# Performance work log

Hardware: AMD Instinct MI355X
Metric: run time of the kernel (lower is better)

The kernel has to match this reference:

```python
import jax, jax.numpy as jnp
import numpy as np

H_RES, W_RES = 32, 32
DIM = 512
NUM_HEADS = 16
HEAD_DIM = DIM // NUM_HEADS
SCALE = HEAD_DIM ** -0.5
B = 16
N = H_RES * W_RES
TABLE_SIZE = (2 * H_RES - 1) * (2 * W_RES - 1)


def _relative_position_index():
    coords_h = np.arange(H_RES)
    coords_w = np.arange(W_RES)
    coords = np.stack(np.meshgrid(coords_h, coords_w, indexing='ij'))  # [2, H, W]
    coords_flat = coords.reshape(2, -1)  # [2, N]
    rel = coords_flat[:, :, None] - coords_flat[:, None, :]  # [2, N, N]
    rel = rel.transpose(1, 2, 0).astype(np.int64)  # [N, N, 2]
    rel[:, :, 0] += H_RES - 1
    rel[:, :, 1] += W_RES - 1
    rel[:, :, 0] *= 2 * W_RES - 1
    return rel.sum(-1)  # [N, N]


def setup_inputs() -> dict:
    key = jax.random.key(0)
    ks = jax.random.split(key, 6)
    x = jax.random.normal(ks[0], (B, N, DIM), dtype=jnp.float32)
    w_qkv = jax.random.normal(ks[1], (DIM, 3 * DIM), dtype=jnp.float32) * (DIM ** -0.5)
    b_qkv = jnp.zeros((3 * DIM,), dtype=jnp.float32)
    w_proj = jax.random.normal(ks[2], (DIM, DIM), dtype=jnp.float32) * (DIM ** -0.5)
    b_proj = jnp.zeros((DIM,), dtype=jnp.float32)
    bias_table = jax.random.normal(ks[3], (TABLE_SIZE, NUM_HEADS), dtype=jnp.float32) * 0.02
    rel_index = jnp.asarray(_relative_position_index(), dtype=jnp.int32)
    return {"x": x, "w_qkv": w_qkv, "b_qkv": b_qkv, "w_proj": w_proj,
            "b_proj": b_proj, "bias_table": bias_table, "rel_index": rel_index}


def reference(x, w_qkv, b_qkv, w_proj, b_proj, bias_table, rel_index):
    Bq, Nq, C = x.shape
    qkv = x @ w_qkv + b_qkv  # [B, N, 3C]
    qkv = qkv.reshape(Bq, Nq, 3, NUM_HEADS, HEAD_DIM)
    q = qkv[:, :, 0].transpose(0, 2, 1, 3) * SCALE  # [B, nH, N, d]
    k = qkv[:, :, 1].transpose(0, 2, 1, 3)
    v = qkv[:, :, 2].transpose(0, 2, 1, 3)
    attn = jnp.einsum('bhnd,bhmd->bhnm', q, k)  # [B, nH, N, N]
    bias = bias_table[rel_index]  # [N, N, nH]
    attn = attn + bias.transpose(2, 0, 1)[None]  # broadcast over batch
    attn = jax.nn.softmax(attn, axis=-1)
    out = jnp.einsum('bhnm,bhmd->bhnd', attn, v)  # [B, nH, N, d]
    out = out.transpose(0, 2, 1, 3).reshape(Bq, Nq, C)
    return out @ w_proj + b_proj
```

## Files before the change

### kernel.cpp

```cpp
#include <hip/hip_runtime.h>
#include <hip/hip_bf16.h>
#include <cstdint>
#include <cstddef>

typedef _Float16 f16;
typedef __attribute__((ext_vector_type(8))) _Float16 f16x8;
typedef __attribute__((ext_vector_type(4))) _Float16 f16x4v;
typedef __bf16 bf16;
typedef __attribute__((ext_vector_type(4))) float f32x4;
typedef __attribute__((ext_vector_type(16))) float f32x16;

#define LOG2E 1.4426950408889634f
#define QK_SCALE 0.17677669529663687f

__device__ __forceinline__ f32x4 mfma16f(f16x8 a, f16x8 b, f32x4 c) {
  return __builtin_amdgcn_mfma_f32_16x16x32_f16(a, b, c, 0, 0, 0);
}
__device__ __forceinline__ f32x16 mfma32f(f16x8 a, f16x8 b, f32x16 c) {
  return __builtin_amdgcn_mfma_f32_32x32x16_f16(a, b, c, 0, 0, 0);
}
__device__ __forceinline__ float exp2_hw(float x) {
  float r; asm("v_exp_f32 %0, %1" : "=v"(r) : "v"(x)); return r;
}
__device__ __forceinline__ uint32_t cvtpk_f16(float a, float b) {
  uint32_t r; asm("v_cvt_pkrtz_f16_f32 %0, %1, %2" : "=v"(r) : "v"(a), "v"(b)); return r;
}
__device__ __forceinline__ void pl32swap(uint32_t& a, uint32_t& b) {
  asm("v_permlane32_swap_b32 %0, %1" : "+v"(a), "+v"(b));
}
__device__ __forceinline__ float lo16f(uint32_t u) { return __uint_as_float(u << 16); }
__device__ __forceinline__ float hi16f(uint32_t u) { return __uint_as_float(u & 0xFFFF0000u); }

__device__ __forceinline__ uint32_t packoff(int m, int k) {
  return (((uint32_t)(m >> 7) * 16u + (uint32_t)(k >> 5)) * 8u + (uint32_t)((m >> 4) & 7)) * 512u
       + (uint32_t)((k >> 3) & 3) * 128u + (uint32_t)(m & 15) * 8u + (uint32_t)(k & 7);
}

__global__ __launch_bounds__(256) void prep_kernel(
    const float* __restrict__ x, const float* __restrict__ wqkv, const float* __restrict__ wproj,
    f16* __restrict__ Xp, f16* __restrict__ Wq, f16* __restrict__ Wp)
{
  const int X4 = 16384 * 512 / 4;
  int e = blockIdx.x * 256 + threadIdx.x;
  if (e < X4) {
    int m = e >> 7, k4 = e & 127;
    f32x4 v = *(const f32x4*)(x + (size_t)e * 4);
    f16x4v o;
    #pragma unroll
    for (int j = 0; j < 4; ++j) o[j] = (f16)v[j];
    *(f16x4v*)(Xp + packoff(m, k4 * 4)) = o;
  } else if (e < X4 + 1536 * 512) {
    int e2 = e - X4;
    int n = e2 >> 9, k = e2 & 511;
    Wq[packoff(n, k)] = (f16)wqkv[k * 1536 + n];
  } else {
    int e3 = e - (X4 + 1536 * 512);
    if (e3 < 512 * 512) {
      int n = e3 >> 9, k = e3 & 511;
      Wp[packoff(n, k)] = (f16)wproj[k * 512 + n];
    }
  }
}

__global__ __launch_bounds__(256) void tblT_kernel(
    const float* __restrict__ btab, float* __restrict__ tblT)
{
  int e = blockIdx.x * 256 + threadIdx.x;
  if (e < 3969 * 16) {
    int h = e & 15, i = e >> 4;
    tblT[h * 4000 + i] = btab[e] * LOG2E;
  }
}

__global__ __launch_bounds__(256) void bias_kernel(
    const float* __restrict__ tblT, bf16* __restrict__ biasM)
{
  int t = blockIdx.x * 256 + threadIdx.x;
  int lane = t & 63;
  int kvb  = (t >> 6) & 31;
  int qb   = (t >> 11) & 31;
  int h    = t >> 16;
  int lq = lane & 31, hi5 = lane >> 5;
  int q = qb * 32 + lq;
  int base = ((q >> 5) + 31) * 63 + (q & 31) + 31 - kvb * 63;
  const float* tp = tblT + h * 4000 + base;
  bf16 outv[16];
  #pragma unroll
  for (int r = 0; r < 16; ++r) {
    int s = (r & 3) + 8 * (r >> 2) + 4 * hi5;
    outv[r] = (bf16)tp[-s];
  }
  *(uint4*)(biasM + (size_t)t * 16) = *(uint4*)&outv[0];
  *(uint4*)(biasM + (size_t)t * 16 + 8) = *(uint4*)&outv[8];
}

template<int NB>
__global__ __launch_bounds__(256) void gemm_frag(
    const f16* __restrict__ Ap, const f16* __restrict__ Bp,
    const float* __restrict__ bvec,
    f16* __restrict__ Qp, f16* __restrict__ Kp, f16* __restrict__ Vt,
    float* __restrict__ out)
{
  const int bid = blockIdx.x;
  const int xcd = bid & 7, idx = bid >> 3;
  int mb, nb;
  if (NB == 12) { int q = idx / 12; mb = xcd * 16 + q; nb = idx - q * 12; }
  else          { mb = xcd * 16 + (idx >> 2); nb = idx & 3; }
  const int tid = threadIdx.x, lane = tid & 63, wave = tid >> 6;
  const int l15 = lane & 15, l4 = lane >> 4;
  const int wr = wave >> 1, wc = wave & 1;

  const f16* pA = Ap + (uint32_t)mb * 65536u + (uint32_t)wr * 2048u + (uint32_t)lane * 8u;
  const f16* pB = Bp + (uint32_t)nb * 65536u + (uint32_t)wc * 2048u + (uint32_t)lane * 8u;

  f16x8 aA[4], bA[4], aB[4], bB[4];
  #pragma unroll
  for (int f = 0; f < 4; ++f) {
    aA[f] = *(const f16x8*)(pA + f * 512);
    bA[f] = *(const f16x8*)(pB + f * 512);
  }
  __builtin_amdgcn_sched_barrier(0);
  #pragma unroll
  for (int f = 0; f < 4; ++f) {
    aB[f] = *(const f16x8*)(pA + 4096 + f * 512);
    bB[f] = *(const f16x8*)(pB + 4096 + f * 512);
  }
  __builtin_amdgcn_sched_barrier(0);
  pA += 8192; pB += 8192;

  f32x4 acc[4][4];
  #pragma unroll
  for (int i = 0; i < 4; ++i)
    #pragma unroll
    for (int j = 0; j < 4; ++j) acc[i][j] = (f32x4){0.f, 0.f, 0.f, 0.f};

  #pragma unroll 1
  for (int it = 0; it < 8; ++it) {
    asm volatile("s_waitcnt vmcnt(8)" ::: "memory");
    #pragma unroll
    for (int mf = 0; mf < 4; ++mf)
      #pragma unroll
      for (int nf = 0; nf < 4; ++nf)
        acc[mf][nf] = mfma16f(aA[mf], bA[nf], acc[mf][nf]);
    #pragma unroll
    for (int f = 0; f < 4; ++f) {
      aA[f] = *(const f16x8*)(pA + f * 512);
      bA[f] = *(const f16x8*)(pB + f * 512);
    }
    __builtin_amdgcn_sched_barrier(0);
    asm volatile("s_waitcnt vmcnt(8)" ::: "memory");
    #pragma unroll
    for (int mf = 0; mf < 4; ++mf)
      #pragma unroll
      for (int nf = 0; nf < 4; ++nf)
        acc[mf][nf] = mfma16f(aB[mf], bB[nf], acc[mf][nf]);
    #pragma unroll
    for (int f = 0; f < 4; ++f) {
      aB[f] = *(const f16x8*)(pA + 4096 + f * 512);
      bB[f] = *(const f16x8*)(pB + 4096 + f * 512);
    }
    __builtin_amdgcn_sched_barrier(0);
    pA += 8192; pB += 8192;
  }

  #pragma unroll
  for (int mf = 0; mf < 4; ++mf) {
    #pragma unroll
    for (int nf = 0; nf < 4; ++nf) {
      int colb = nb * 128 + wc * 64 + nf * 16 + l15;
      float bb = bvec[colb];
      #pragma unroll
      for (int i = 0; i < 4; ++i) {
        int m = mb * 128 + wr * 64 + mf * 16 + l4 * 4 + i;
        float v = acc[mf][nf][i] + bb;
        if (NB == 4) {
          out[(size_t)m * 512 + colb] = v;
        } else {
          int t = colb >> 9, cc = colb & 511;
          int b = m >> 10, n = m & 1023;
          int hh = cc >> 5, d = cc & 31;
          int bh2 = b * 16 + hh;
          if (t == 0) {
            v *= (QK_SCALE * LOG2E);
            uint32_t off = (((uint32_t)bh2 * 32u + (uint32_t)(n >> 5)) * 2u + (uint32_t)(d >> 4)) * 512u
                         + ((uint32_t)((d >> 3) & 1) * 32u + (uint32_t)(n & 31)) * 8u + (uint32_t)(d & 7);
            Qp[off] = (f16)v;
          } else if (t == 1) {
            Kp[((size_t)(bh2 * 2 + (d >> 4)) * 1024 + n) * 16 + (d & 15)] = (f16)v;
          } else {
            Vt[((size_t)(bh2 * 128 + (n >> 3)) * 32 + d) * 8 + (n & 7)] = (f16)v;
          }
        }
      }
    }
  }
}

__global__ __launch_bounds__(256) void attn_kernel(
    const f16* __restrict__ Qp, const f16* __restrict__ Kp, const f16* __restrict__ Vt,
    const bf16* __restrict__ biasM, f16* __restrict__ Op)
{
  const int bid = blockIdx.x;
  const int xcd = bid & 7, slot = bid >> 3;
  const int h = xcd * 2 + (slot >> 6);
  const int rest = slot & 63;
  const int qg = rest >> 4, b = rest & 15;
  const int bh = b * 16 + h;
  const int tid = threadIdx.x, lane = tid & 63, wave = tid >> 6;
  const int lq = lane & 31, hi5 = lane >> 5;

  const int qb0 = qg * 8 + wave * 2;
  const int m0 = b * 1024 + qb0 * 32;

  const uint32_t qbase = ((uint32_t)bh * 32u + (uint32_t)qb0) * 1024u + (uint32_t)lane * 8u;
  const f16x8 q00 = *(const f16x8*)(Qp + qbase);
  const f16x8 q01 = *(const f16x8*)(Qp + qbase + 512);
  const f16x8 q10 = *(const f16x8*)(Qp + qbase + 1024);
  const f16x8 q11 = *(const f16x8*)(Qp + qbase + 1536);

  uint32_t koff = (uint32_t)bh * 32768u + (uint32_t)lq * 16u + (uint32_t)hi5 * 8u;
  uint32_t voff = (uint32_t)bh * 32768u + (uint32_t)hi5 * 256u + (uint32_t)lq * 8u;
  uint32_t boff = ((uint32_t)h * 32u + (uint32_t)qb0) * 32768u + (uint32_t)lane * 16u;

  f16x8 kA0 = *(const f16x8*)(Kp + koff);
  f16x8 kA1 = *(const f16x8*)(Kp + koff + 16384);
  uint4 p0A = *(const uint4*)(biasM + boff);
  uint4 p1A = *(const uint4*)(biasM + boff + 8);
  uint4 p2A = *(const uint4*)(biasM + boff + 32768);
  uint4 p3A = *(const uint4*)(biasM + boff + 32768 + 8);
  f16x8 vA0 = *(const f16x8*)(Vt + voff);
  f16x8 vA1 = *(const f16x8*)(Vt + voff + 512);
  f16x8 kB0 = *(const f16x8*)(Kp + koff + 512);
  f16x8 kB1 = *(const f16x8*)(Kp + koff + 16384 + 512);
  uint4 p0B = *(const uint4*)(biasM + boff + 1024);
  uint4 p1B = *(const uint4*)(biasM + boff + 1024 + 8);
  uint4 p2B = *(const uint4*)(biasM + boff + 32768 + 1024);
  uint4 p3B = *(const uint4*)(biasM + boff + 32768 + 1024 + 8);
  f16x8 vB0 = *(const f16x8*)(Vt + voff + 1024);
  f16x8 vB1 = *(const f16x8*)(Vt + voff + 1536);

  f32x16 O0, O1;
  #pragma unroll
  for (int i = 0; i < 16; ++i) { O0[i] = 0.f; O1[i] = 0.f; }
  f32x4 racc0 = {0.f, 0.f, 0.f, 0.f}, racc1 = {0.f, 0.f, 0.f, 0.f};

  union Uf { uint32_t u[4]; f16x8 v; };

#define UNPACK16(S, Pa, Pb)                              \
  S[0]  = lo16f(Pa.x); S[1]  = hi16f(Pa.x);              \
  S[2]  = lo16f(Pa.y); S[3]  = hi16f(Pa.y);              \
  S[4]  = lo16f(Pa.z); S[5]  = hi16f(Pa.z);              \
  S[6]  = lo16f(Pa.w); S[7]  = hi16f(Pa.w);              \
  S[8]  = lo16f(Pb.x); S[9]  = hi16f(Pb.x);              \
  S[10] = lo16f(Pb.y); S[11] = hi16f(Pb.y);              \
  S[12] = lo16f(Pb.z); S[13] = hi16f(Pb.z);              \
  S[14] = lo16f(Pb.w); S[15] = hi16f(Pb.w);

  auto tile = [&](f16x8& K0, f16x8& K1, f16x8& V0, f16x8& V1,
                  uint4& P0, uint4& P1, uint4& P2, uint4& P3,
                  uint32_t kpre, uint32_t vpre, uint32_t bpre) {
    asm volatile("s_waitcnt vmcnt(8)" ::: "memory");
    f32x16 S0, S1;
    UNPACK16(S0, P0, P1)
    UNPACK16(S1, P2, P3)
    S0 = mfma32f(K0, q00, S0);
    S0 = mfma32f(K1, q01, S0);
    S1 = mfma32f(K0, q10, S1);
    S1 = mfma32f(K1, q11, S1);
    K0 = *(const f16x8*)(Kp + koff + kpre);
    K1 = *(const f16x8*)(Kp + koff + 16384 + kpre);
    P0 = *(const uint4*)(biasM + boff + bpre);
    P1 = *(const uint4*)(biasM + boff + bpre + 8);
    P2 = *(const uint4*)(biasM + boff + 32768 + bpre);
    P3 = *(const uint4*)(biasM + boff + 32768 + bpre + 8);
    __builtin_amdgcn_sched_barrier(0);
    {
      float e0  = exp2_hw(S0[0]),  e1  = exp2_hw(S0[1]),  e2  = exp2_hw(S0[2]),  e3  = exp2_hw(S0[3]);
      float e4  = exp2_hw(S0[4]),  e5  = exp2_hw(S0[5]),  e6  = exp2_hw(S0[6]),  e7  = exp2_hw(S0[7]);
      float e8  = exp2_hw(S0[8]),  e9  = exp2_hw(S0[9]),  e10 = exp2_hw(S0[10]), e11 = exp2_hw(S0[11]);
      float e12 = exp2_hw(S0[12]), e13 = exp2_hw(S0[13]), e14 = exp2_hw(S0[14]), e15 = exp2_hw(S0[15]);
      racc0[0] += e0 + e4;   racc0[1] += e1 + e5;
      racc0[2] += e2 + e6;   racc0[3] += e3 + e7;
      racc0[0] += e8 + e12;  racc0[1] += e9 + e13;
      racc0[2] += e10 + e14; racc0[3] += e11 + e15;
      uint32_t u0 = cvtpk_f16(e0,  e1),  u1 = cvtpk_f16(e2,  e3);
      uint32_t u2 = cvtpk_f16(e4,  e5),  u3 = cvtpk_f16(e6,  e7);
      uint32_t u4 = cvtpk_f16(e8,  e9),  u5 = cvtpk_f16(e10, e11);
      uint32_t u6 = cvtpk_f16(e12, e13), u7 = cvtpk_f16(e14, e15);
      pl32swap(u0, u2); pl32swap(u1, u3); pl32swap(u4, u6); pl32swap(u5, u7);
      Uf a1; a1.u[0] = u0; a1.u[1] = u1; a1.u[2] = u2; a1.u[3] = u3;
      Uf a2; a2.u[0] = u4; a2.u[1] = u5; a2.u[2] = u6; a2.u[3] = u7;
      O0 = mfma32f(a1.v, V0, O0);
      O0 = mfma32f(a2.v, V1, O0);
    }
    {
      float e0  = exp2_hw(S1[0]),  e1  = exp2_hw(S1[1]),  e2  = exp2_hw(S1[2]),  e3  = exp2_hw(S1[3]);
      float e4  = exp2_hw(S1[4]),  e5  = exp2_hw(S1[5]),  e6  = exp2_hw(S1[6]),  e7  = exp2_hw(S1[7]);
      float e8  = exp2_hw(S1[8]),  e9  = exp2_hw(S1[9]),  e10 = exp2_hw(S1[10]), e11 = exp2_hw(S1[11]);
      float e12 = exp2_hw(S1[12]), e13 = exp2_hw(S1[13]), e14 = exp2_hw(S1[14]), e15 = exp2_hw(S1[15]);
      racc1[0] += e0 + e4;   racc1[1] += e1 + e5;
      racc1[2] += e2 + e6;   racc1[3] += e3 + e7;
      racc1[0] += e8 + e12;  racc1[1] += e9 + e13;
      racc1[2] += e10 + e14; racc1[3] += e11 + e15;
      uint32_t u0 = cvtpk_f16(e0,  e1),  u1 = cvtpk_f16(e2,  e3);
      uint32_t u2 = cvtpk_f16(e4,  e5),  u3 = cvtpk_f16(e6,  e7);
      uint32_t u4 = cvtpk_f16(e8,  e9),  u5 = cvtpk_f16(e10, e11);
      uint32_t u6 = cvtpk_f16(e12, e13), u7 = cvtpk_f16(e14, e15);
      pl32swap(u0, u2); pl32swap(u1, u3); pl32swap(u4, u6); pl32swap(u5, u7);
      Uf a1; a1.u[0] = u0; a1.u[1] = u1; a1.u[2] = u2; a1.u[3] = u3;
      Uf a2; a2.u[0] = u4; a2.u[1] = u5; a2.u[2] = u6; a2.u[3] = u7;
      O1 = mfma32f(a1.v, V0, O1);
      O1 = mfma32f(a2.v, V1, O1);
    }
    V0 = *(const f16x8*)(Vt + voff + vpre);
    V1 = *(const f16x8*)(Vt + voff + vpre + 512);
    __builtin_amdgcn_sched_barrier(0);
  };

  #pragma unroll 1
  for (int it = 0; it < 16; ++it) {
    tile(kA0, kA1, vA0, vA1, p0A, p1A, p2A, p3A, 1024u, 2048u, 2048u);
    tile(kB0, kB1, vB0, vB1, p0B, p1B, p2B, p3B, 1536u, 3072u, 3072u);
    koff += 1024u; voff += 2048u; boff += 2048u;
  }

  float rs0 = (racc0[0] + racc0[1]) + (racc0[2] + racc0[3]);
  rs0 += __shfl_xor(rs0, 32);
  float inv0 = 1.0f / rs0;
  float rs1 = (racc1[0] + racc1[1]) + (racc1[2] + racc1[3]);
  rs1 += __shfl_xor(rs1, 32);
  float inv1 = 1.0f / rs1;

  const int kcol = h * 32 + lq;
  #pragma unroll
  for (int r = 0; r < 16; ++r) {
    int qrow = (r & 3) + 8 * (r >> 2) + 4 * hi5;
    float t0 = __shfl(inv0, qrow);
    float t1 = __shfl(inv1, qrow);
    Op[packoff(m0 + qrow, kcol)] = (f16)(O0[r] * t0);
    Op[packoff(m0 + 32 + qrow, kcol)] = (f16)(O1[r] * t1);
  }
}

extern "C" void kernel_launch(void* const* d_in, const int* in_sizes, int n_in,
                              void* d_out, int out_size, void* d_ws, size_t ws_size,
                              hipStream_t stream) {
  const float* x     = (const float*)d_in[0];
  const float* wqkv  = (const float*)d_in[1];
  const float* bqkv  = (const float*)d_in[2];
  const float* wproj = (const float*)d_in[3];
  const float* bproj = (const float*)d_in[4];
  const float* btab  = (const float*)d_in[5];
  float* out = (float*)d_out;

  char* ws = (char*)d_ws;
  size_t off = 0;
  auto walloc = [&](size_t bytes) {
    void* p = ws + off;
    off += (bytes + 255) & ~(size_t)255;
    return p;
  };
  const size_t PAD = 262144;
  f16* Xp   = (f16*)walloc((size_t)16384 * 512 * 2 + PAD);
  f16* Wq   = (f16*)walloc((size_t)1536 * 512 * 2 + PAD);
  f16* Wp   = (f16*)walloc((size_t)512 * 512 * 2 + PAD);
  float* tblT = (float*)walloc((size_t)16 * 4000 * 4);
  f16* Qp   = (f16*)walloc((size_t)16384 * 512 * 2 + PAD);
  f16* Kp   = (f16*)walloc((size_t)16384 * 512 * 2 + PAD);
  f16* Vt   = (f16*)walloc((size_t)16384 * 512 * 2 + PAD);
  bf16* biasM = (bf16*)walloc((size_t)16 * 1024 * 1024 * 2 + PAD);
  f16* Op   = (f16*)walloc((size_t)16384 * 512 * 2 + PAD);

  const int prep_total = 16384 * 512 / 4 + 1536 * 512 + 512 * 512;
  prep_kernel<<<(prep_total + 255) / 256, 256, 0, stream>>>(
      x, wqkv, wproj, Xp, Wq, Wp);

  tblT_kernel<<<(3969 * 16 + 255) / 256, 256, 0, stream>>>(btab, tblT);

  bias_kernel<<<4096, 256, 0, stream>>>(tblT, biasM);

  gemm_frag<12><<<1536, 256, 0, stream>>>(
      Xp, Wq, bqkv, Qp, Kp, Vt, nullptr);

  attn_kernel<<<1024, 256, 0, stream>>>(Qp, Kp, Vt, biasM, Op);

  gemm_frag<4><<<512, 256, 0, stream>>>(
      Op, Wp, bproj, nullptr, nullptr, nullptr, out);
}
```

Baseline: 181.3 us.

## Compress bias to Toeplitz rows, LDS-stage GEMM, and MFMA row sums

Three changes land together. The full per-head N×N bias matrix (32 MB bf16) is replaced by a compact table of 63 block-diagonal slices per head, which the attention kernel indexes with a decreasing pointer, so bias reads come from a small, cache-resident buffer instead of HBM. The GEMM now stages A and B tiles through a triple-buffered LDS ring using global_load_lds, with barriers, instead of direct register loads. The softmax row sums are computed by extra MFMAs against a ones vector rather than VALU adds and shuffles. The costs are extra LDS barriers in the GEMM and doubled MFMA work for the row sums.

Result: faster. 169.7 us (-6.4%).

```diff
diff --git a/kernel.cpp b/kernel.cpp
--- a/kernel.cpp
+++ b/kernel.cpp
@@ -30,6 +30,12 @@
 }
 __device__ __forceinline__ float lo16f(uint32_t u) { return __uint_as_float(u << 16); }
 __device__ __forceinline__ float hi16f(uint32_t u) { return __uint_as_float(u & 0xFFFF0000u); }
+
+__device__ __forceinline__ void gl16(const f16* g, f16* l) {
+  __builtin_amdgcn_global_load_lds(
+      (const __attribute__((address_space(1))) void*)g,
+      (__attribute__((address_space(3))) void*)l, 16, 0, 0);
+}
 
 __device__ __forceinline__ uint32_t packoff(int m, int k) {
   return (((uint32_t)(m >> 7) * 16u + (uint32_t)(k >> 5)) * 8u + (uint32_t)((m >> 4) & 7)) * 512u
@@ -72,26 +78,24 @@
   }
 }
 
-__global__ __launch_bounds__(256) void bias_kernel(
-    const float* __restrict__ tblT, bf16* __restrict__ biasM)
+__global__ __launch_bounds__(256) void biasC_kernel(
+    const float* __restrict__ tblT, bf16* __restrict__ biasC)
 {
   int t = blockIdx.x * 256 + threadIdx.x;
+  if (t >= 16 * 63 * 64) return;
   int lane = t & 63;
-  int kvb  = (t >> 6) & 31;
-  int qb   = (t >> 11) & 31;
-  int h    = t >> 16;
+  int sh = t >> 6;
+  int s = sh % 63, h = sh / 63;
   int lq = lane & 31, hi5 = lane >> 5;
-  int q = qb * 32 + lq;
-  int base = ((q >> 5) + 31) * 63 + (q & 31) + 31 - kvb * 63;
-  const float* tp = tblT + h * 4000 + base;
-  bf16 outv[16];
+  const float* row = tblT + h * 4000 + s * 63 + 31 + lq;
+  bf16 o[16];
   #pragma unroll
   for (int r = 0; r < 16; ++r) {
-    int s = (r & 3) + 8 * (r >> 2) + 4 * hi5;
-    outv[r] = (bf16)tp[-s];
-  }
-  *(uint4*)(biasM + (size_t)t * 16) = *(uint4*)&outv[0];
-  *(uint4*)(biasM + (size_t)t * 16 + 8) = *(uint4*)&outv[8];
+    int kx = (r & 3) + 8 * (r >> 2) + 4 * hi5;
+    o[r] = (bf16)row[-kx];
+  }
+  *(uint4*)(biasC + (size_t)t * 16) = *(uint4*)&o[0];
+  *(uint4*)(biasC + (size_t)t * 16 + 8) = *(uint4*)&o[8];
 }
 
 template<int NB>
@@ -101,6 +105,8 @@
     f16* __restrict__ Qp, f16* __restrict__ Kp, f16* __restrict__ Vt,
     float* __restrict__ out)
 {
+  __shared__ f16 sA[3][4096];
+  __shared__ f16 sB[3][4096];
   const int bid = blockIdx.x;
   const int xcd = bid & 7, idx = bid >> 3;
   int mb, nb;
@@ -110,23 +116,18 @@
   const int l15 = lane & 15, l4 = lane >> 4;
   const int wr = wave >> 1, wc = wave & 1;
 
-  const f16* pA = Ap + (uint32_t)mb * 65536u + (uint32_t)wr * 2048u + (uint32_t)lane * 8u;
-  const f16* pB = Bp + (uint32_t)nb * 65536u + (uint32_t)wc * 2048u + (uint32_t)lane * 8u;
-
-  f16x8 aA[4], bA[4], aB[4], bB[4];
-  #pragma unroll
-  for (int f = 0; f < 4; ++f) {
-    aA[f] = *(const f16x8*)(pA + f * 512);
-    bA[f] = *(const f16x8*)(pB + f * 512);
-  }
-  __builtin_amdgcn_sched_barrier(0);
-  #pragma unroll
-  for (int f = 0; f < 4; ++f) {
-    aB[f] = *(const f16x8*)(pA + 4096 + f * 512);
-    bB[f] = *(const f16x8*)(pB + 4096 + f * 512);
-  }
-  __builtin_amdgcn_sched_barrier(0);
-  pA += 8192; pB += 8192;
+  const f16* gA = Ap + (uint32_t)mb * 65536u + (uint32_t)wave * 1024u + (uint32_t)lane * 8u;
+  const f16* gB = Bp + (uint32_t)nb * 65536u + (uint32_t)wave * 1024u + (uint32_t)lane * 8u;
+  const int wl = wave * 1024;
+
+  gl16(gA,        &sA[0][wl]);
+  gl16(gA + 512,  &sA[0][wl + 512]);
+  gl16(gB,        &sB[0][wl]);
+  gl16(gB + 512,  &sB[0][wl + 512]);
+  gl16(gA + 4096, &sA[1][wl]);
+  gl16(gA + 4608, &sA[1][wl + 512]);
+  gl16(gB + 4096, &sB[1][wl]);
+  gl16(gB + 4608, &sB[1][wl + 512]);
 
   f32x4 acc[4][4];
   #pragma unroll
@@ -134,34 +135,34 @@
     #pragma unroll
     for (int j = 0; j < 4; ++j) acc[i][j] = (f32x4){0.f, 0.f, 0.f, 0.f};
 
-  #pragma unroll 1
-  for (int it = 0; it < 8; ++it) {
+  const uint32_t aoff = (uint32_t)(wr * 4) * 512u + (uint32_t)lane * 8u;
+  const uint32_t boff = (uint32_t)(wc * 4) * 512u + (uint32_t)lane * 8u;
+
+  #pragma unroll
+  for (int kt = 0; kt < 16; ++kt) {
+    const int s2 = (kt + 2) % 3;
+    gl16(gA + (kt + 2) * 4096,       &sA[s2][wl]);
+    gl16(gA + (kt + 2) * 4096 + 512, &sA[s2][wl + 512]);
+    gl16(gB + (kt + 2) * 4096,       &sB[s2][wl]);
+    gl16(gB + (kt + 2) * 4096 + 512, &sB[s2][wl + 512]);
     asm volatile("s_waitcnt vmcnt(8)" ::: "memory");
+    asm volatile("s_barrier" ::: "memory");
+    const int s0 = kt % 3;
+    f16x8 af[4], bfr[4];
+    #pragma unroll
+    for (int f = 0; f < 4; ++f) {
+      af[f]  = *(const f16x8*)&sA[s0][aoff + f * 512];
+      bfr[f] = *(const f16x8*)&sB[s0][boff + f * 512];
+    }
+    asm volatile("s_waitcnt lgkmcnt(0)" ::: "memory");
+    asm volatile("s_barrier" ::: "memory");
     #pragma unroll
     for (int mf = 0; mf < 4; ++mf)
       #pragma unroll
       for (int nf = 0; nf < 4; ++nf)
-        acc[mf][nf] = mfma16f(aA[mf], bA[nf], acc[mf][nf]);
-    #pragma unroll
-    for (int f = 0; f < 4; ++f) {
-      aA[f] = *(const f16x8*)(pA + f * 512);
-      bA[f] = *(const f16x8*)(pB + f * 512);
-    }
-    __builtin_amdgcn_sched_barrier(0);
-    asm volatile("s_waitcnt vmcnt(8)" ::: "memory");
-    #pragma unroll
-    for (int mf = 0; mf < 4; ++mf)
-      #pragma unroll
-      for (int nf = 0; nf < 4; ++nf)
-        acc[mf][nf] = mfma16f(aB[mf], bB[nf], acc[mf][nf]);
-    #pragma unroll
-    for (int f = 0; f < 4; ++f) {
-      aB[f] = *(const f16x8*)(pA + 4096 + f * 512);
-      bB[f] = *(const f16x8*)(pB + 4096 + f * 512);
-    }
-    __builtin_amdgcn_sched_barrier(0);
-    pA += 8192; pB += 8192;
-  }
+        acc[mf][nf] = mfma16f(af[mf], bfr[nf], acc[mf][nf]);
+  }
+  asm volatile("s_waitcnt vmcnt(0)" ::: "memory");
 
   #pragma unroll
   for (int mf = 0; mf < 4; ++mf) {
@@ -198,7 +199,7 @@
 
 __global__ __launch_bounds__(256) void attn_kernel(
     const f16* __restrict__ Qp, const f16* __restrict__ Kp, const f16* __restrict__ Vt,
-    const bf16* __restrict__ biasM, f16* __restrict__ Op)
+    const bf16* __restrict__ biasC, f16* __restrict__ Op)
 {
   const int bid = blockIdx.x;
   const int xcd = bid & 7, slot = bid >> 3;
@@ -220,29 +221,32 @@
 
   uint32_t koff = (uint32_t)bh * 32768u + (uint32_t)lq * 16u + (uint32_t)hi5 * 8u;
   uint32_t voff = (uint32_t)bh * 32768u + (uint32_t)hi5 * 256u + (uint32_t)lq * 8u;
-  uint32_t boff = ((uint32_t)h * 32u + (uint32_t)qb0) * 32768u + (uint32_t)lane * 16u;
+  const bf16* bp = biasC + ((uint32_t)(h * 63 + qb0 + 31) * 64u + (uint32_t)lane) * 16u;
 
   f16x8 kA0 = *(const f16x8*)(Kp + koff);
   f16x8 kA1 = *(const f16x8*)(Kp + koff + 16384);
-  uint4 p0A = *(const uint4*)(biasM + boff);
-  uint4 p1A = *(const uint4*)(biasM + boff + 8);
-  uint4 p2A = *(const uint4*)(biasM + boff + 32768);
-  uint4 p3A = *(const uint4*)(biasM + boff + 32768 + 8);
+  uint4 p0A = *(const uint4*)(bp);
+  uint4 p1A = *(const uint4*)(bp + 8);
+  uint4 p2A = *(const uint4*)(bp + 1024);
+  uint4 p3A = *(const uint4*)(bp + 1032);
   f16x8 vA0 = *(const f16x8*)(Vt + voff);
   f16x8 vA1 = *(const f16x8*)(Vt + voff + 512);
   f16x8 kB0 = *(const f16x8*)(Kp + koff + 512);
   f16x8 kB1 = *(const f16x8*)(Kp + koff + 16384 + 512);
-  uint4 p0B = *(const uint4*)(biasM + boff + 1024);
-  uint4 p1B = *(const uint4*)(biasM + boff + 1024 + 8);
-  uint4 p2B = *(const uint4*)(biasM + boff + 32768 + 1024);
-  uint4 p3B = *(const uint4*)(biasM + boff + 32768 + 1024 + 8);
+  uint4 p0B = *(const uint4*)(bp - 1024);
+  uint4 p1B = *(const uint4*)(bp - 1016);
+  uint4 p2B = *(const uint4*)(bp);
+  uint4 p3B = *(const uint4*)(bp + 8);
   f16x8 vB0 = *(const f16x8*)(Vt + voff + 1024);
   f16x8 vB1 = *(const f16x8*)(Vt + voff + 1536);
 
-  f32x16 O0, O1;
-  #pragma unroll
-  for (int i = 0; i < 16; ++i) { O0[i] = 0.f; O1[i] = 0.f; }
-  f32x4 racc0 = {0.f, 0.f, 0.f, 0.f}, racc1 = {0.f, 0.f, 0.f, 0.f};
+  f32x16 O0, O1, R0, R1;
+  #pragma unroll
+  for (int i = 0; i < 16; ++i) { O0[i] = 0.f; O1[i] = 0.f; R0[i] = 0.f; R1[i] = 0.f; }
+
+  f16x8 onesv;
+  { union { uint32_t u[4]; f16x8 v; } c;
+    c.u[0] = c.u[1] = c.u[2] = c.u[3] = 0x3C003C00u; onesv = c.v; }
 
   union Uf { uint32_t u[4]; f16x8 v; };
 
@@ -258,7 +262,7 @@
 
   auto tile = [&](f16x8& K0, f16x8& K1, f16x8& V0, f16x8& V1,
                   uint4& P0, uint4& P1, uint4& P2, uint4& P3,
-                  uint32_t kpre, uint32_t vpre, uint32_t bpre) {
+                  uint32_t kpre, uint32_t vpre, int bpre) {
     asm volatile("s_waitcnt vmcnt(8)" ::: "memory");
     f32x16 S0, S1;
     UNPACK16(S0, P0, P1)
@@ -269,20 +273,16 @@
     S1 = mfma32f(K1, q11, S1);
     K0 = *(const f16x8*)(Kp + koff + kpre);
     K1 = *(const f16x8*)(Kp + koff + 16384 + kpre);
-    P0 = *(const uint4*)(biasM + boff + bpre);
-    P1 = *(const uint4*)(biasM + boff + bpre + 8);
-    P2 = *(const uint4*)(biasM + boff + 32768 + bpre);
-    P3 = *(const uint4*)(biasM + boff + 32768 + bpre + 8);
+    P0 = *(const uint4*)(bp + bpre);
+    P1 = *(const uint4*)(bp + bpre + 8);
+    P2 = *(const uint4*)(bp + bpre + 1024);
+    P3 = *(const uint4*)(bp + bpre + 1032);
     __builtin_amdgcn_sched_barrier(0);
     {
       float e0  = exp2_hw(S0[0]),  e1  = exp2_hw(S0[1]),  e2  = exp2_hw(S0[2]),  e3  = exp2_hw(S0[3]);
       float e4  = exp2_hw(S0[4]),  e5  = exp2_hw(S0[5]),  e6  = exp2_hw(S0[6]),  e7  = exp2_hw(S0[7]);
       float e8  = exp2_hw(S0[8]),  e9  = exp2_hw(S0[9]),  e10 = exp2_hw(S0[10]), e11 = exp2_hw(S0[11]);
       float e12 = exp2_hw(S0[12]), e13 = exp2_hw(S0[13]), e14 = exp2_hw(S0[14]), e15 = exp2_hw(S0[15]);
-      racc0[0] += e0 + e4;   racc0[1] += e1 + e5;
-      racc0[2] += e2 + e6;   racc0[3] += e3 + e7;
-      racc0[0] += e8 + e12;  racc0[1] += e9 + e13;
-      racc0[2] += e10 + e14; racc0[3] += e11 + e15;
       uint32_t u0 = cvtpk_f16(e0,  e1),  u1 = cvtpk_f16(e2,  e3);
       uint32_t u2 = cvtpk_f16(e4,  e5),  u3 = cvtpk_f16(e6,  e7);
       uint32_t u4 = cvtpk_f16(e8,  e9),  u5 = cvtpk_f16(e10, e11);
@@ -292,16 +292,14 @@
       Uf a2; a2.u[0] = u4; a2.u[1] = u5; a2.u[2] = u6; a2.u[3] = u7;
       O0 = mfma32f(a1.v, V0, O0);
       O0 = mfma32f(a2.v, V1, O0);
+      R0 = mfma32f(a1.v, onesv, R0);
+      R0 = mfma32f(a2.v, onesv, R0);
     }
     {
       float e0  = exp2_hw(S1[0]),  e1  = exp2_hw(S1[1]),  e2  = exp2_hw(S1[2]),  e3  = exp2_hw(S1[3]);
       float e4  = exp2_hw(S1[4]),  e5  = exp2_hw(S1[5]),  e6  = exp2_hw(S1[6]),  e7  = exp2_hw(S1[7]);
       float e8  = exp2_hw(S1[8]),  e9  = exp2_hw(S1[9]),  e10 = exp2_hw(S1[10]), e11 = exp2_hw(S1[11]);
       float e12 = exp2_hw(S1[12]), e13 = exp2_hw(S1[13]), e14 = exp2_hw(S1[14]), e15 = exp2_hw(S1[15]);
-      racc1[0] += e0 + e4;   racc1[1] += e1 + e5;
-      racc1[2] += e2 + e6;   racc1[3] += e3 + e7;
-      racc1[0] += e8 + e12;  racc1[1] += e9 + e13;
-      racc1[2] += e10 + e14; racc1[3] += e11 + e15;
       uint32_t u0 = cvtpk_f16(e0,  e1),  u1 = cvtpk_f16(e2,  e3);
       uint32_t u2 = cvtpk_f16(e4,  e5),  u3 = cvtpk_f16(e6,  e7);
       uint32_t u4 = cvtpk_f16(e8,  e9),  u5 = cvtpk_f16(e10, e11);
@@ -311,6 +309,8 @@
       Uf a2; a2.u[0] = u4; a2.u[1] = u5; a2.u[2] = u6; a2.u[3] = u7;
       O1 = mfma32f(a1.v, V0, O1);
       O1 = mfma32f(a2.v, V1, O1);
+      R1 = mfma32f(a1.v, onesv, R1);
+      R1 = mfma32f(a2.v, onesv, R1);
     }
     V0 = *(const f16x8*)(Vt + voff + vpre);
     V1 = *(const f16x8*)(Vt + voff + vpre + 512);
@@ -319,26 +319,17 @@
 
   #pragma unroll 1
   for (int it = 0; it < 16; ++it) {
-    tile(kA0, kA1, vA0, vA1, p0A, p1A, p2A, p3A, 1024u, 2048u, 2048u);
-    tile(kB0, kB1, vB0, vB1, p0B, p1B, p2B, p3B, 1536u, 3072u, 3072u);
-    koff += 1024u; voff += 2048u; boff += 2048u;
-  }
-
-  float rs0 = (racc0[0] + racc0[1]) + (racc0[2] + racc0[3]);
-  rs0 += __shfl_xor(rs0, 32);
-  float inv0 = 1.0f / rs0;
-  float rs1 = (racc1[0] + racc1[1]) + (racc1[2] + racc1[3]);
-  rs1 += __shfl_xor(rs1, 32);
-  float inv1 = 1.0f / rs1;
+    tile(kA0, kA1, vA0, vA1, p0A, p1A, p2A, p3A, 1024u, 2048u, -2048);
+    tile(kB0, kB1, vB0, vB1, p0B, p1B, p2B, p3B, 1536u, 3072u, -3072);
+    koff += 1024u; voff += 2048u; bp -= 2048;
+  }
 
   const int kcol = h * 32 + lq;
   #pragma unroll
   for (int r = 0; r < 16; ++r) {
     int qrow = (r & 3) + 8 * (r >> 2) + 4 * hi5;
-    float t0 = __shfl(inv0, qrow);
-    float t1 = __shfl(inv1, qrow);
-    Op[packoff(m0 + qrow, kcol)] = (f16)(O0[r] * t0);
-    Op[packoff(m0 + 32 + qrow, kcol)] = (f16)(O1[r] * t1);
+    Op[packoff(m0 + qrow, kcol)] = (f16)(O0[r] / R0[r]);
+    Op[packoff(m0 + 32 + qrow, kcol)] = (f16)(O1[r] / R1[r]);
   }
 }
 
@@ -368,7 +359,7 @@
   f16* Qp   = (f16*)walloc((size_t)16384 * 512 * 2 + PAD);
   f16* Kp   = (f16*)walloc((size_t)16384 * 512 * 2 + PAD);
   f16* Vt   = (f16*)walloc((size_t)16384 * 512 * 2 + PAD);
-  bf16* biasM = (bf16*)walloc((size_t)16 * 1024 * 1024 * 2 + PAD);
+  bf16* biasC = (bf16*)walloc((size_t)16 * 63 * 64 * 16 * 2 + PAD);
   f16* Op   = (f16*)walloc((size_t)16384 * 512 * 2 + PAD);
 
   const int prep_total = 16384 * 512 / 4 + 1536 * 512 + 512 * 512;
@@ -377,12 +368,12 @@
 
   tblT_kernel<<<(3969 * 16 + 255) / 256, 256, 0, stream>>>(btab, tblT);
 
-  bias_kernel<<<4096, 256, 0, stream>>>(tblT, biasM);
+  biasC_kernel<<<(16 * 63 * 64 + 255) / 256, 256, 0, stream>>>(tblT, biasC);
 
   gemm_frag<12><<<1536, 256, 0, stream>>>(
       Xp, Wq, bqkv, Qp, Kp, Vt, nullptr);
 
-  attn_kernel<<<1024, 256, 0, stream>>>(Qp, Kp, Vt, biasM, Op);
+  attn_kernel<<<1024, 256, 0, stream>>>(Qp, Kp, Vt, biasC, Op);
 
   gemm_frag<4><<<512, 256, 0, stream>>>(
       Op, Wp, bproj, nullptr, nullptr, nullptr, out);
```
